# Optimization experiments

Measured on AMD Instinct MI355X. Metric: run time of the kernel, lower is better.

The kernel has to match this reference:

```python
import jax, jax.numpy as jnp
import numpy as np

D_MODEL = 1024
N_HEADS = 16
HEAD_DIM = D_MODEL // N_HEADS
B, S = 4, 2048


def setup_inputs() -> dict:
    key = jax.random.key(0)
    ks = jax.random.split(key, 12)
    s = 1.0 / np.sqrt(D_MODEL)
    inp = {
        'query': jax.random.normal(ks[0], (B, S, D_MODEL), jnp.float32),
        'key': jax.random.normal(ks[1], (B, S, D_MODEL), jnp.float32),
        'value': jax.random.normal(ks[2], (B, S, D_MODEL), jnp.float32),
        # causal mask, broadcast over batch and heads: [1,1,S,S]
        'mask': jnp.tril(jnp.ones((S, S), jnp.int32))[None, None],
        'Wq': jax.random.normal(ks[3], (D_MODEL, D_MODEL), jnp.float32) * s,
        'bq': jnp.zeros((D_MODEL,), jnp.float32),
        'Wk': jax.random.normal(ks[4], (D_MODEL, D_MODEL), jnp.float32) * s,
        'bk': jnp.zeros((D_MODEL,), jnp.float32),
        'Wv': jax.random.normal(ks[5], (D_MODEL, D_MODEL), jnp.float32) * s,
        'bv': jnp.zeros((D_MODEL,), jnp.float32),
        'Wo': jax.random.normal(ks[6], (D_MODEL, D_MODEL), jnp.float32) * s,
        'bo': jnp.zeros((D_MODEL,), jnp.float32),
    }
    return inp


def reference(query, key, value, mask, Wq, bq, Wk, bk, Wv, bv, Wo, bo):
    b, q_len, _ = query.shape
    scale = jnp.sqrt(jnp.float32(HEAD_DIM))
    # projections
    q = query @ Wq + bq
    k = key @ Wk + bk
    v = value @ Wv + bv
    # [b, h, s, hd]
    q = q.reshape(b, q_len, N_HEADS, HEAD_DIM).transpose(0, 2, 1, 3)
    k = k.reshape(b, -1, N_HEADS, HEAD_DIM).transpose(0, 2, 1, 3)
    v = v.reshape(b, -1, N_HEADS, HEAD_DIM).transpose(0, 2, 1, 3)
    scores = jnp.einsum('bhqd,bhkd->bhqk', q, k) / scale
    scores = jnp.where(mask == 0, jnp.float32(-jnp.inf), scores)
    attn = jax.nn.softmax(scores, axis=-1)  # dropout p=0 / eval mode
    out = jnp.einsum('bhqk,bhkd->bhqd', attn, v)
    out = out.transpose(0, 2, 1, 3).reshape(b, q_len, D_MODEL)
    return out @ Wo + bo
```

## Files before the change

kernel.cpp:

```cpp
#include <hip/hip_runtime.h>
#include <hip/hip_bf16.h>

typedef __attribute__((ext_vector_type(8))) short short8;
typedef __attribute__((ext_vector_type(4))) float floatx4;
typedef __attribute__((ext_vector_type(4))) unsigned short ushort4v;

#define D_MODEL 1024
#define S_LEN   2048
#define N_HEADS 16
#define HEAD_DIM 64
#define BATCH   4

__device__ __forceinline__ unsigned short f2bf(float x) {
    union { float f; unsigned int u; } v; v.f = x;
    unsigned int u = v.u;
    unsigned int r = (u + 0x7FFFu + ((u >> 16) & 1u)) >> 16;
    return (unsigned short)r;
}
__device__ __forceinline__ unsigned short f2bf_trunc(float x) {
    union { float f; unsigned int u; } v; v.f = x;
    return (unsigned short)(v.u >> 16);
}

__device__ __forceinline__ void gload_lds16(const void* g, void* s) {
    __builtin_amdgcn_global_load_lds(
        (const __attribute__((address_space(1))) void*)g,
        (__attribute__((address_space(3))) void*)s, 16, 0, 0);
}

struct Conv3 {
    const float* src[3];
    unsigned short* dst[3];
};

__global__ __launch_bounds__(256) void conv_bf16(Conv3 a) {
    const float* s = a.src[blockIdx.z];
    unsigned short* d = a.dst[blockIdx.z];
    size_t i = ((size_t)blockIdx.x * 256 + threadIdx.x) * 8;
    float4 f0 = *(const float4*)(s + i);
    float4 f1 = *(const float4*)(s + i + 4);
    short8 v;
    v[0] = (short)f2bf(f0.x); v[1] = (short)f2bf(f0.y);
    v[2] = (short)f2bf(f0.z); v[3] = (short)f2bf(f0.w);
    v[4] = (short)f2bf(f1.x); v[5] = (short)f2bf(f1.y);
    v[6] = (short)f2bf(f1.z); v[7] = (short)f2bf(f1.w);
    *(short8*)(d + i) = v;
}

struct Trans4 {
    const float* W[4];
    unsigned short* Wt[4];
};

__global__ __launch_bounds__(256) void transpose_w(Trans4 args) {
    __shared__ unsigned short tile[32][33];
    const float* W = args.W[blockIdx.z];
    unsigned short* Wt = args.Wt[blockIdx.z];
    int n0 = blockIdx.x * 32;
    int k0 = blockIdx.y * 32;
    int t = threadIdx.x;
    int r = t >> 5, c = t & 31;
    for (int i = 0; i < 4; ++i) {
        int k = k0 + r + i * 8;
        tile[r + i * 8][c] = f2bf(W[(size_t)k * D_MODEL + n0 + c]);
    }
    __syncthreads();
    for (int i = 0; i < 4; ++i) {
        int n = n0 + r + i * 8;
        Wt[(size_t)n * D_MODEL + k0 + c] = tile[c][r + i * 8];
    }
}

struct GemmIn {
    const unsigned short* A;
    const unsigned short* Bt;
    const float* bias;
    void* C;
    int mode;
};
struct Gemm3 { GemmIn g[3]; };

#define BAR()   asm volatile("s_barrier" ::: "memory")
#define LGKM0() asm volatile("s_waitcnt lgkmcnt(0)" ::: "memory")
#define VMW2()  asm volatile("s_waitcnt vmcnt(2)" ::: "memory")
#define VMW0()  asm volatile("s_waitcnt vmcnt(0)" ::: "memory")

#define READ_A4(BUF)                                                           \
    _Pragma("unroll") for (int ii = 0; ii < 4; ++ii) {                         \
        aF[ii][0] = *(const short8*)&lds[(BUF)*16384 + aOff + ii*512];         \
        aF[ii][1] = *(const short8*)&lds[(BUF)*16384 + aOff + ii*512 + 4096];  \
    }
#define READ_B2(BUF, J0, DST)                                                  \
    _Pragma("unroll") for (int jj = 0; jj < 2; ++jj) {                         \
        DST[jj][0] = *(const short8*)&lds[(BUF)*16384 + bOff + ((J0)+jj)*512]; \
        DST[jj][1] = *(const short8*)&lds[(BUF)*16384 + bOff + ((J0)+jj)*512 + 4096]; \
    }
#define MFMA_H(J0, BREG)                                                       \
    __builtin_amdgcn_s_setprio(1);                                             \
    _Pragma("unroll") for (int ii = 0; ii < 4; ++ii)                           \
    _Pragma("unroll") for (int jj = 0; jj < 2; ++jj) {                         \
        acc[ii][(J0)+jj] = __builtin_amdgcn_mfma_f32_16x16x32_bf16(            \
            aF[ii][0], BREG[jj][0], acc[ii][(J0)+jj], 0, 0, 0);                \
        acc[ii][(J0)+jj] = __builtin_amdgcn_mfma_f32_16x16x32_bf16(            \
            aF[ii][1], BREG[jj][1], acc[ii][(J0)+jj], 0, 0, 0);                \
    }                                                                          \
    __builtin_amdgcn_s_setprio(0)

__global__ __launch_bounds__(256, 2) void gemm_128(Gemm3 args) {
    constexpr int K = D_MODEL, N = D_MODEL;
    constexpr int NT = K / 64;
    constexpr int NI = NT / 2;
    GemmIn g = args.g[blockIdx.z];

    __shared__ __align__(16) unsigned short lds[32768];

    const int m0 = blockIdx.x * 128;
    const int n0 = blockIdx.y * 128;
    const int t = threadIdx.x;
    const int w = t >> 6, lane = t & 63;
    const int quad = lane >> 4, l16 = lane & 15;
    const int wm = w >> 1, wn = w & 1;

    const int srow = w * 32 + (lane >> 2);
    const int scol = ((lane & 3) * 8) ^ ((lane & 32) ? 16 : 0);

    const int fx = (quad * 8) ^ ((l16 & 8) ? 16 : 0);
    const int aOff = (wm * 64 + l16) * 32 + fx;
    const int bOff = 8192 + (wn * 64 + l16) * 32 + fx;

    floatx4 acc[4][4] = {};
    short8 aF[4][2], bE[2][2], bO[2][2];

    auto stageA = [&](int buf, int kt) {
        const unsigned short* s0 = g.A + (size_t)(m0 + srow) * K + kt * 64 + scol;
        unsigned short* d0 = &lds[buf * 16384 + (w * 32) * 32];
        gload_lds16(s0, d0);
        gload_lds16(s0 + 32, d0 + 4096);
        gload_lds16(s0 + (size_t)16 * K, d0 + 512);
        gload_lds16(s0 + (size_t)16 * K + 32, d0 + 512 + 4096);
    };
    auto stageB = [&](int buf, int kt) {
        const unsigned short* s0 = g.Bt + (size_t)(n0 + srow) * K + kt * 64 + scol;
        unsigned short* d0 = &lds[buf * 16384 + 8192 + (w * 32) * 32];
        gload_lds16(s0, d0);
        gload_lds16(s0 + 32, d0 + 4096);
        gload_lds16(s0 + (size_t)16 * K, d0 + 512);
        gload_lds16(s0 + (size_t)16 * K + 32, d0 + 512 + 4096);
    };

    stageA(0, 0); stageB(0, 0);
    VMW0();
    BAR();

    for (int n = 0; n < NI - 1; ++n) {
        const int t0 = 2 * n;
        READ_A4(0); READ_B2(0, 0, bE);
        stageB(1, t0 + 1);
        BAR(); LGKM0();
        MFMA_H(0, bE);
        BAR();
        READ_B2(0, 2, bO);
        stageA(1, t0 + 1);
        BAR(); LGKM0();
        MFMA_H(2, bO);
        VMW0();
        BAR();
        READ_A4(1); READ_B2(1, 0, bE);
        stageB(0, t0 + 2);
        BAR(); LGKM0();
        MFMA_H(0, bE);
        BAR();
        READ_B2(1, 2, bO);
        stageA(0, t0 + 2);
        BAR(); LGKM0();
        MFMA_H(2, bO);
        VMW0();
        BAR();
    }

    {
        READ_A4(0); READ_B2(0, 0, bE);
        stageB(1, NT - 1);
        BAR(); LGKM0();
        MFMA_H(0, bE);
        BAR();
        READ_B2(0, 2, bO);
        stageA(1, NT - 1);
        BAR(); LGKM0();
        MFMA_H(2, bO);
        VMW0();
        BAR();
        READ_A4(1); READ_B2(1, 0, bE);
        BAR(); LGKM0();
        MFMA_H(0, bE);
        BAR();
        READ_B2(1, 2, bO);
        LGKM0();
        MFMA_H(2, bO);
    }

    if (g.mode == 2) {
        unsigned short* Ct = (unsigned short*)g.C;
#pragma unroll
        for (int j = 0; j < 4; ++j) {
            int col = n0 + wn * 64 + j * 16 + l16;
            int h = col >> 6, dd = col & 63;
            float bv = g.bias[col];
#pragma unroll
            for (int i = 0; i < 4; ++i) {
                int row0 = m0 + wm * 64 + i * 16 + quad * 4;
                int bb = row0 >> 11, s = row0 & 2047;
                ushort4v u;
#pragma unroll
                for (int r = 0; r < 4; ++r) u[r] = f2bf(acc[i][j][r] + bv);
                *(ushort4v*)(Ct + ((size_t)(bb * 16 + h) * 64 + dd) * 2048 + s) = u;
            }
        }
    } else {
#pragma unroll
        for (int j = 0; j < 4; ++j) {
            int col = n0 + wn * 64 + j * 16 + l16;
            float bv = g.bias[col];
#pragma unroll
            for (int i = 0; i < 4; ++i) {
#pragma unroll
                for (int r = 0; r < 4; ++r) {
                    int row = m0 + wm * 64 + i * 16 + quad * 4 + r;
                    float v = acc[i][j][r] + bv;
                    if (g.mode == 1)
                        ((float*)g.C)[(size_t)row * N + col] = v;
                    else
                        ((unsigned short*)g.C)[(size_t)row * N + col] = f2bf(v);
                }
            }
        }
    }
}

__global__ __launch_bounds__(512) void flash_attn(
    const unsigned short* __restrict__ Qp,
    const unsigned short* __restrict__ Kp,
    const unsigned short* __restrict__ Vtg,
    unsigned short* __restrict__ Op) {
    constexpr int S = S_LEN, D = D_MODEL;
    __shared__ __align__(16) unsigned short Ks[2 * 4096];
    __shared__ __align__(16) unsigned short Vs[2 * 4096];
    __shared__ __align__(16) unsigned short Ps[8][1024];

    int pair = blockIdx.x;
    int bh = blockIdx.y;
    int b = bh >> 4;
    int t = threadIdx.x;
    int wave = t >> 6, lane = t & 63;
    int quad = lane >> 4, l16 = lane & 15;

    const size_t head_off = (size_t)b * S * D + (size_t)(bh & 15) * HEAD_DIM;
    const unsigned short* Khead = Kp + head_off;
    const unsigned short* Vhead = Vtg + (size_t)bh * 64 * S;

    int q0l = pair * 128, q0h = (15 - pair) * 128;
    int qgl = q0l + wave * 16 + l16;
    int qgh = q0h + wave * 16 + l16;

    const unsigned short* qpl = Qp + head_off + (size_t)qgl * D + quad * 8;
    short8 ql0 = *(const short8*)qpl, ql1 = *(const short8*)(qpl + 32);
    const unsigned short* qph = Qp + head_off + (size_t)qgh * D + quad * 8;
    short8 qh0 = *(const short8*)qph, qh1 = *(const short8*)(qph + 32);

    floatx4 ol[4] = {}, oh[4] = {};
    float ll = 0.f, lh = 0.f;
    const float cs = 0.125f * 1.44269504088896340736f;

    int sw = wave & 3;
    bool doK = wave < 4;
    int srow = sw * 16 + (lane >> 2);
    int scol = ((lane & 3) * 8) ^ ((lane & 32) ? 16 : 0);

    auto stage = [&](int buf, int k0) {
        if (doK) {
            const unsigned short* s0 = Khead + (size_t)(k0 + srow) * D + scol;
            unsigned short* d0 = Ks + buf * 4096 + sw * 512;
            gload_lds16(s0, d0);
            gload_lds16(s0 + 32, d0 + 2048);
        } else {
            const unsigned short* s0 = Vhead + (size_t)srow * S + k0 + scol;
            unsigned short* d0 = Vs + buf * 4096 + sw * 512;
            gload_lds16(s0, d0);
            gload_lds16(s0 + 32, d0 + 2048);
        }
    };

    int wqminl = q0l + wave * 16, wqmaxl = wqminl + 15;
    int wqminh = q0h + wave * 16, wqmaxh = wqminh + 15;

    const int swz = (quad * 8) ^ ((l16 & 8) ? 16 : 0);
    const int pswz = (l16 & 8) ? 16 : 0;
    unsigned short* pw = &Ps[wave][0];

    auto half_step = [&](const unsigned short* Kb, const unsigned short* Vb,
                         int k0, int qg, int wqmin, float& l_i,
                         floatx4* o, short8 qb0, short8 qb1) {
        floatx4 st[4];
        __builtin_amdgcn_s_setprio(1);
        for (int gk = 0; gk < 4; ++gk) {
            short8 ka0 = *(const short8*)&Kb[(gk * 16 + l16) * 32 + swz];
            short8 ka1 = *(const short8*)&Kb[2048 + (gk * 16 + l16) * 32 + swz];
            floatx4 s = {};
            s = __builtin_amdgcn_mfma_f32_16x16x32_bf16(ka0, qb0, s, 0, 0, 0);
            s = __builtin_amdgcn_mfma_f32_16x16x32_bf16(ka1, qb1, s, 0, 0, 0);
            st[gk] = s;
        }
        __builtin_amdgcn_s_setprio(0);

        float sv[16];
        float rs = 0.f;
        if (k0 + 63 < wqmin) {
            for (int i = 0; i < 16; ++i) {
                sv[i] = __builtin_amdgcn_exp2f(st[i >> 2][i & 3] * cs);
                rs += sv[i];
            }
        } else {
            for (int gk = 0; gk < 4; ++gk)
                for (int r = 0; r < 4; ++r) {
                    int key = k0 + gk * 16 + quad * 4 + r;
                    float p = (key <= qg)
                        ? __builtin_amdgcn_exp2f(st[gk][r] * cs) : 0.f;
                    sv[gk * 4 + r] = p;
                    rs += p;
                }
        }
        rs += __shfl_xor(rs, 16);
        rs += __shfl_xor(rs, 32);
        l_i += rs;

        for (int gk = 0; gk < 4; ++gk) {
            ushort4v u;
            for (int r = 0; r < 4; ++r) u[r] = f2bf_trunc(sv[gk * 4 + r]);
            *(ushort4v*)&pw[(gk >> 1) * 512 + l16 * 32 +
                            ((((gk & 1) * 16) + quad * 4) ^ pswz)] = u;
        }

        short8 pf0 = *(const short8*)&pw[l16 * 32 + swz];
        short8 pf1 = *(const short8*)&pw[512 + l16 * 32 + swz];
        __builtin_amdgcn_s_setprio(1);
        for (int jd = 0; jd < 4; ++jd) {
            short8 va0 = *(const short8*)&Vb[(jd * 16 + l16) * 32 + swz];
            short8 va1 = *(const short8*)&Vb[2048 + (jd * 16 + l16) * 32 + swz];
            o[jd] = __builtin_amdgcn_mfma_f32_16x16x32_bf16(va0, pf0, o[jd], 0, 0, 0);
            o[jd] = __builtin_amdgcn_mfma_f32_16x16x32_bf16(va1, pf1, o[jd], 0, 0, 0);
        }
        __builtin_amdgcn_s_setprio(0);
    };

    int n_kt = 2 * (15 - pair) + 2;
    stage(0, 0);
    for (int kt = 0; kt < n_kt; ++kt) {
        int k0 = kt * 64;
        if (kt + 1 < n_kt) {
            stage((kt + 1) & 1, k0 + 64);
            VMW2();
        } else {
            VMW0();
        }
        BAR();

        const unsigned short* Kb = Ks + (kt & 1) * 4096;
        const unsigned short* Vb = Vs + (kt & 1) * 4096;
        if (k0 <= wqmaxl) half_step(Kb, Vb, k0, qgl, wqminl, ll, ol, ql0, ql1);
        if (k0 <= wqmaxh) half_step(Kb, Vb, k0, qgh, wqminh, lh, oh, qh0, qh1);
        BAR();
    }

    {
        float inv = 1.0f / ll;
        unsigned short* op = Op + head_off + (size_t)qgl * D;
        for (int jd = 0; jd < 4; ++jd) {
            ushort4v u;
            for (int r = 0; r < 4; ++r) u[r] = f2bf(ol[jd][r] * inv);
            *(ushort4v*)(op + jd * 16 + quad * 4) = u;
        }
    }
    {
        float inv = 1.0f / lh;
        unsigned short* op = Op + head_off + (size_t)qgh * D;
        for (int jd = 0; jd < 4; ++jd) {
            ushort4v u;
            for (int r = 0; r < 4; ++r) u[r] = f2bf(oh[jd][r] * inv);
            *(ushort4v*)(op + jd * 16 + quad * 4) = u;
        }
    }
}

extern "C" void kernel_launch(void* const* d_in, const int* in_sizes, int n_in,
                              void* d_out, int out_size, void* d_ws,
                              size_t ws_size, hipStream_t stream) {
    const float* query = (const float*)d_in[0];
    const float* key   = (const float*)d_in[1];
    const float* value = (const float*)d_in[2];
    const float* Wq = (const float*)d_in[4];
    const float* bq = (const float*)d_in[5];
    const float* Wk = (const float*)d_in[6];
    const float* bk = (const float*)d_in[7];
    const float* Wv = (const float*)d_in[8];
    const float* bv = (const float*)d_in[9];
    const float* Wo = (const float*)d_in[10];
    const float* bo = (const float*)d_in[11];
    float* out = (float*)d_out;

    char* ws = (char*)d_ws;
    const size_t WT_SZ = (size_t)D_MODEL * D_MODEL * 2;
    const size_t X_SZ = (size_t)BATCH * S_LEN * D_MODEL * 2;
    unsigned short* wtq = (unsigned short*)(ws);
    unsigned short* wtk = (unsigned short*)(ws + WT_SZ);
    unsigned short* wtv = (unsigned short*)(ws + 2 * WT_SZ);
    unsigned short* wto = (unsigned short*)(ws + 3 * WT_SZ);
    unsigned short* Qbf = (unsigned short*)(ws + 4 * WT_SZ);
    unsigned short* Kbf = (unsigned short*)(ws + 4 * WT_SZ + X_SZ);
    unsigned short* Vbf = (unsigned short*)(ws + 4 * WT_SZ + 2 * X_SZ);
    unsigned short* Qp  = (unsigned short*)(ws + 4 * WT_SZ + 3 * X_SZ);
    unsigned short* Kp  = (unsigned short*)(ws + 4 * WT_SZ + 4 * X_SZ);
    unsigned short* Vtg = (unsigned short*)(ws + 4 * WT_SZ + 5 * X_SZ);
    unsigned short* Ao  = Qbf;

    Trans4 ta;
    ta.W[0] = Wq; ta.W[1] = Wk; ta.W[2] = Wv; ta.W[3] = Wo;
    ta.Wt[0] = wtq; ta.Wt[1] = wtk; ta.Wt[2] = wtv; ta.Wt[3] = wto;
    transpose_w<<<dim3(32, 32, 4), 256, 0, stream>>>(ta);

    Conv3 ca;
    ca.src[0] = query; ca.src[1] = key; ca.src[2] = value;
    ca.dst[0] = Qbf;   ca.dst[1] = Kbf; ca.dst[2] = Vbf;
    conv_bf16<<<dim3(4096, 1, 3), 256, 0, stream>>>(ca);

    Gemm3 gq;
    gq.g[0].A = Qbf; gq.g[0].Bt = wtq; gq.g[0].bias = bq; gq.g[0].C = Qp;  gq.g[0].mode = 0;
    gq.g[1].A = Kbf; gq.g[1].Bt = wtk; gq.g[1].bias = bk; gq.g[1].C = Kp;  gq.g[1].mode = 0;
    gq.g[2].A = Vbf; gq.g[2].Bt = wtv; gq.g[2].bias = bv; gq.g[2].C = Vtg; gq.g[2].mode = 2;
    gemm_128<<<dim3(64, 8, 3), 256, 0, stream>>>(gq);

    flash_attn<<<dim3(8, BATCH * N_HEADS), 512, 0, stream>>>(
        Qp, Kp, Vtg, Ao);

    Gemm3 go;
    go.g[0].A = Ao; go.g[0].Bt = wto; go.g[0].bias = bo; go.g[0].C = out; go.g[0].mode = 1;
    gemm_128<<<dim3(64, 8, 1), 256, 0, stream>>>(go);
}
```

Before: 304.8 us.

## Fold softmax scale into Q projection, MFMA row sums, triple-buffer K/V

The softmax scale (1/sqrt(d)·log2e) moves into the Q projection epilogue, so each score no longer needs a multiply before exp2. Row sums of P are computed with an extra MFMA against a ones vector instead of adds and cross-lane shuffles. K/V staging goes from double to triple buffering with a deeper vmcnt wait, and blocks are remapped so neighbouring blocks share heads. The trade-off is more LDS per block, two extra MFMAs per step, and Q stored in bf16 after scaling.

```diff
diff --git a/kernel.cpp b/kernel.cpp
--- a/kernel.cpp
+++ b/kernel.cpp
@@ -77,11 +77,13 @@
     const float* bias;
     void* C;
     int mode;
+    float scale;
 };
 struct Gemm3 { GemmIn g[3]; };
 
 #define BAR()   asm volatile("s_barrier" ::: "memory")
 #define LGKM0() asm volatile("s_waitcnt lgkmcnt(0)" ::: "memory")
+#define VMW4()  asm volatile("s_waitcnt vmcnt(4)" ::: "memory")
 #define VMW2()  asm volatile("s_waitcnt vmcnt(2)" ::: "memory")
 #define VMW0()  asm volatile("s_waitcnt vmcnt(0)" ::: "memory")
 
@@ -212,7 +214,7 @@
                 int bb = row0 >> 11, s = row0 & 2047;
                 ushort4v u;
 #pragma unroll
-                for (int r = 0; r < 4; ++r) u[r] = f2bf(acc[i][j][r] + bv);
+                for (int r = 0; r < 4; ++r) u[r] = f2bf((acc[i][j][r] + bv) * g.scale);
                 *(ushort4v*)(Ct + ((size_t)(bb * 16 + h) * 64 + dd) * 2048 + s) = u;
             }
         }
@@ -226,7 +228,7 @@
 #pragma unroll
                 for (int r = 0; r < 4; ++r) {
                     int row = m0 + wm * 64 + i * 16 + quad * 4 + r;
-                    float v = acc[i][j][r] + bv;
+                    float v = (acc[i][j][r] + bv) * g.scale;
                     if (g.mode == 1)
                         ((float*)g.C)[(size_t)row * N + col] = v;
                     else
@@ -243,12 +245,13 @@
     const unsigned short* __restrict__ Vtg,
     unsigned short* __restrict__ Op) {
     constexpr int S = S_LEN, D = D_MODEL;
-    __shared__ __align__(16) unsigned short Ks[2 * 4096];
-    __shared__ __align__(16) unsigned short Vs[2 * 4096];
+    __shared__ __align__(16) unsigned short Ks[3 * 4096];
+    __shared__ __align__(16) unsigned short Vs[3 * 4096];
     __shared__ __align__(16) unsigned short Ps[8][1024];
 
-    int pair = blockIdx.x;
-    int bh = blockIdx.y;
+    int id = blockIdx.x + (blockIdx.y << 3);
+    int pair = (id >> 3) & 7;
+    int bh = (id & 7) | ((id >> 6) << 3);
     int b = bh >> 4;
     int t = threadIdx.x;
     int wave = t >> 6, lane = t & 63;
@@ -268,8 +271,11 @@
     short8 qh0 = *(const short8*)qph, qh1 = *(const short8*)(qph + 32);
 
     floatx4 ol[4] = {}, oh[4] = {};
-    float ll = 0.f, lh = 0.f;
-    const float cs = 0.125f * 1.44269504088896340736f;
+    floatx4 lsl = {}, lsh = {};
+
+    short8 a1;
+#pragma unroll
+    for (int e = 0; e < 8; ++e) a1[e] = (l16 == 0) ? (short)0x3F80 : (short)0;
 
     int sw = wave & 3;
     bool doK = wave < 4;
@@ -298,7 +304,7 @@
     unsigned short* pw = &Ps[wave][0];
 
     auto half_step = [&](const unsigned short* Kb, const unsigned short* Vb,
-                         int k0, int qg, int wqmin, float& l_i,
+                         int k0, int qg, int wqmin, floatx4& ls,
                          floatx4* o, short8 qb0, short8 qb1) {
         floatx4 st[4];
         __builtin_amdgcn_s_setprio(1);
@@ -313,25 +319,17 @@
         __builtin_amdgcn_s_setprio(0);
 
         float sv[16];
-        float rs = 0.f;
         if (k0 + 63 < wqmin) {
-            for (int i = 0; i < 16; ++i) {
-                sv[i] = __builtin_amdgcn_exp2f(st[i >> 2][i & 3] * cs);
-                rs += sv[i];
-            }
+            for (int i = 0; i < 16; ++i)
+                sv[i] = __builtin_amdgcn_exp2f(st[i >> 2][i & 3]);
         } else {
             for (int gk = 0; gk < 4; ++gk)
                 for (int r = 0; r < 4; ++r) {
                     int key = k0 + gk * 16 + quad * 4 + r;
-                    float p = (key <= qg)
-                        ? __builtin_amdgcn_exp2f(st[gk][r] * cs) : 0.f;
-                    sv[gk * 4 + r] = p;
-                    rs += p;
+                    sv[gk * 4 + r] = (key <= qg)
+                        ? __builtin_amdgcn_exp2f(st[gk][r]) : 0.f;
                 }
         }
-        rs += __shfl_xor(rs, 16);
-        rs += __shfl_xor(rs, 32);
-        l_i += rs;
 
         for (int gk = 0; gk < 4; ++gk) {
             ushort4v u;
@@ -343,6 +341,8 @@
         short8 pf0 = *(const short8*)&pw[l16 * 32 + swz];
         short8 pf1 = *(const short8*)&pw[512 + l16 * 32 + swz];
         __builtin_amdgcn_s_setprio(1);
+        ls = __builtin_amdgcn_mfma_f32_16x16x32_bf16(a1, pf0, ls, 0, 0, 0);
+        ls = __builtin_amdgcn_mfma_f32_16x16x32_bf16(a1, pf1, ls, 0, 0, 0);
         for (int jd = 0; jd < 4; ++jd) {
             short8 va0 = *(const short8*)&Vb[(jd * 16 + l16) * 32 + swz];
             short8 va1 = *(const short8*)&Vb[2048 + (jd * 16 + l16) * 32 + swz];
@@ -354,25 +354,28 @@
 
     int n_kt = 2 * (15 - pair) + 2;
     stage(0, 0);
+    stage(1, 64);
     for (int kt = 0; kt < n_kt; ++kt) {
         int k0 = kt * 64;
-        if (kt + 1 < n_kt) {
-            stage((kt + 1) & 1, k0 + 64);
+        if (kt + 2 < n_kt) {
+            stage((kt + 2) % 3, k0 + 128);
+            VMW4();
+        } else if (kt + 1 < n_kt) {
             VMW2();
         } else {
             VMW0();
         }
         BAR();
 
-        const unsigned short* Kb = Ks + (kt & 1) * 4096;
-        const unsigned short* Vb = Vs + (kt & 1) * 4096;
-        if (k0 <= wqmaxl) half_step(Kb, Vb, k0, qgl, wqminl, ll, ol, ql0, ql1);
-        if (k0 <= wqmaxh) half_step(Kb, Vb, k0, qgh, wqminh, lh, oh, qh0, qh1);
+        const unsigned short* Kb = Ks + (kt % 3) * 4096;
+        const unsigned short* Vb = Vs + (kt % 3) * 4096;
+        if (k0 <= wqmaxl) half_step(Kb, Vb, k0, qgl, wqminl, lsl, ol, ql0, ql1);
+        if (k0 <= wqmaxh) half_step(Kb, Vb, k0, qgh, wqminh, lsh, oh, qh0, qh1);
         BAR();
     }
 
     {
-        float inv = 1.0f / ll;
+        float inv = 1.0f / __shfl(lsl[0], l16);
         unsigned short* op = Op + head_off + (size_t)qgl * D;
         for (int jd = 0; jd < 4; ++jd) {
             ushort4v u;
@@ -381,7 +384,7 @@
         }
     }
     {
-        float inv = 1.0f / lh;
+        float inv = 1.0f / __shfl(lsh[0], l16);
         unsigned short* op = Op + head_off + (size_t)qgh * D;
         for (int jd = 0; jd < 4; ++jd) {
             ushort4v u;
@@ -432,16 +435,17 @@
     ca.dst[0] = Qbf;   ca.dst[1] = Kbf; ca.dst[2] = Vbf;
     conv_bf16<<<dim3(4096, 1, 3), 256, 0, stream>>>(ca);
 
+    const float q_scale = 0.125f * 1.44269504088896340736f;
     Gemm3 gq;
-    gq.g[0].A = Qbf; gq.g[0].Bt = wtq; gq.g[0].bias = bq; gq.g[0].C = Qp;  gq.g[0].mode = 0;
-    gq.g[1].A = Kbf; gq.g[1].Bt = wtk; gq.g[1].bias = bk; gq.g[1].C = Kp;  gq.g[1].mode = 0;
-    gq.g[2].A = Vbf; gq.g[2].Bt = wtv; gq.g[2].bias = bv; gq.g[2].C = Vtg; gq.g[2].mode = 2;
+    gq.g[0].A = Qbf; gq.g[0].Bt = wtq; gq.g[0].bias = bq; gq.g[0].C = Qp;  gq.g[0].mode = 0; gq.g[0].scale = q_scale;
+    gq.g[1].A = Kbf; gq.g[1].Bt = wtk; gq.g[1].bias = bk; gq.g[1].C = Kp;  gq.g[1].mode = 0; gq.g[1].scale = 1.0f;
+    gq.g[2].A = Vbf; gq.g[2].Bt = wtv; gq.g[2].bias = bv; gq.g[2].C = Vtg; gq.g[2].mode = 2; gq.g[2].scale = 1.0f;
     gemm_128<<<dim3(64, 8, 3), 256, 0, stream>>>(gq);
 
     flash_attn<<<dim3(8, BATCH * N_HEADS), 512, 0, stream>>>(
         Qp, Kp, Vtg, Ao);
 
     Gemm3 go;
-    go.g[0].A = Ao; go.g[0].Bt = wto; go.g[0].bias = bo; go.g[0].C = out; go.g[0].mode = 1;
+    go.g[0].A = Ao; go.g[0].Bt = wto; go.g[0].bias = bo; go.g[0].C = out; go.g[0].mode = 1; go.g[0].scale = 1.0f;
     gemm_128<<<dim3(64, 8, 1), 256, 0, stream>>>(go);
 }
```

Result: no change. 306.8 us (+0.7%).
